# Optimization experiments

Measured on AMD Instinct MI355X. Metric: run time of the kernel, lower is better.

Reference implementation:

```python
import jax, jax.numpy as jnp
import numpy as np

N, E, B_GRAPHS = 50000, 512000, 64
XD, ED, C, H, L = 16, 8, 64, 2, 2
EPS = 1e-5


def setup_inputs() -> dict:
    key = jax.random.key(0)
    ks = jax.random.split(key, 20)
    w = lambda k, shape: jax.random.normal(k, shape, jnp.float32) * 0.1
    return {
        "x": jax.random.normal(ks[0], (N, XD), jnp.float32),
        "edge_attr": jax.random.normal(ks[1], (E, ED), jnp.float32),
        "edge_src": jax.random.randint(ks[2], (E,), 0, N, dtype=jnp.int32),
        "edge_dst": jax.random.randint(ks[3], (E,), 0, N, dtype=jnp.int32),
        "batch": jnp.sort(jax.random.randint(ks[4], (N,), 0, B_GRAPHS, dtype=jnp.int32)),
        "node_W": w(ks[5], (XD, C)), "node_b": jnp.zeros((C,), jnp.float32),
        "edge_W": w(ks[6], (ED, C)), "edge_b": jnp.zeros((C,), jnp.float32),
        "Wq": w(ks[7], (L, C, H * C)), "bq": jnp.zeros((L, H * C), jnp.float32),
        "Wk": w(ks[8], (L, C, H * C)), "bk": jnp.zeros((L, H * C), jnp.float32),
        "Wv": w(ks[9], (L, C, H * C)), "bv": jnp.zeros((L, H * C), jnp.float32),
        "We": w(ks[10], (L, C, H * C)), "be": jnp.zeros((L, H * C), jnp.float32),
        "Wskip": w(ks[11], (L, C, C)), "bskip": jnp.zeros((L, C), jnp.float32),
        "gamma": jnp.ones((L, C), jnp.float32), "beta": jnp.zeros((L, C), jnp.float32),
        "gate_W": w(ks[12], (C, 1)), "gate_b": jnp.zeros((1,), jnp.float32),
        "out_W": w(ks[13], (C, 1)), "out_b": jnp.zeros((1,), jnp.float32),
    }


def reference(x, edge_attr, edge_src, edge_dst, batch,
              node_W, node_b, edge_W, edge_b,
              Wq, bq, Wk, bk, Wv, bv, We, be,
              Wskip, bskip, gamma, beta,
              gate_W, gate_b, out_W, out_b):
    n = x.shape[0]
    h = x @ node_W + node_b                       # node encoder: [N, C]
    e = edge_attr @ edge_W + edge_b               # edge encoder: [E, C]
    scale = 1.0 / jnp.sqrt(jnp.float32(C))
    for i in range(L):
        identity = h
        # TransformerConv (UniMP), concat=False -> mean over heads
        q = (h @ Wq[i] + bq[i]).reshape(n, H, C)
        k = (h @ Wk[i] + bk[i]).reshape(n, H, C)
        v = (h @ Wv[i] + bv[i]).reshape(n, H, C)
        ep = (e @ We[i] + be[i]).reshape(-1, H, C)
        k_e = k[edge_src] + ep                    # [E, H, C]
        v_e = v[edge_src] + ep                    # [E, H, C]
        logits = jnp.einsum('ehc,ehc->eh', q[edge_dst], k_e) * scale
        # segment softmax over incoming edges of each target node
        m = jax.ops.segment_max(logits, edge_dst, num_segments=n)
        a = jnp.exp(logits - m[edge_dst])
        denom = jax.ops.segment_sum(a, edge_dst, num_segments=n)
        alpha = a / denom[edge_dst]               # [E, H]
        agg = jax.ops.segment_sum(alpha[:, :, None] * v_e, edge_dst, num_segments=n)
        out = agg.mean(axis=1) + h @ Wskip[i] + bskip[i]   # root/skip term
        # BatchNorm1d (training mode, biased variance)
        mu = out.mean(axis=0)
        var = out.var(axis=0)
        out = gamma[i] * (out - mu) * jax.lax.rsqrt(var + EPS) + beta[i]
        out = jax.nn.leaky_relu(out, 0.01)
        h = out + identity                        # residual
    # GlobalAttention pooling over graphs
    gate = (h @ gate_W + gate_b)[:, 0]            # [N]
    gm = jax.ops.segment_max(gate, batch, num_segments=B_GRAPHS)
    ge = jnp.exp(gate - gm[batch])
    gd = jax.ops.segment_sum(ge, batch, num_segments=B_GRAPHS)
    wts = ge / gd[batch]
    pooled = jax.ops.segment_sum(wts[:, None] * h, batch, num_segments=B_GRAPHS)
    return jax.nn.sigmoid(pooled @ out_W + out_b)  # [B_GRAPHS, 1]
```

## Files before the change

kernel.cpp:

```cpp
#include <hip/hip_runtime.h>
#include <hip/hip_bf16.h>

typedef unsigned short ushort_t;
typedef __attribute__((ext_vector_type(8))) short short8;
typedef __attribute__((ext_vector_type(4))) float float4v;

__device__ __forceinline__ float bfu_lo(unsigned u) {
    return __uint_as_float(u << 16);
}
__device__ __forceinline__ float bfu_hi(unsigned u) {
    return __uint_as_float(u & 0xffff0000u);
}
__device__ __forceinline__ ushort_t f2bf(float f) {
    __hip_bfloat16 h = __float2bfloat16(f);
    return *reinterpret_cast<ushort_t*>(&h);
}



__global__ __launch_bounds__(256) void setup_kernel(
    const float* __restrict__ x, const float* __restrict__ node_W,
    const float* __restrict__ node_b,
    const float* __restrict__ edge_W, const float* __restrict__ edge_b,
    const float* __restrict__ We, const float* __restrict__ be,
    const float* __restrict__ Wq, const float* __restrict__ bq,
    const float* __restrict__ Wk, const float* __restrict__ bk,
    const float* __restrict__ Wv, const float* __restrict__ bv,
    const float* __restrict__ Wskip, const float* __restrict__ bskip,
    float* __restrict__ h, ushort_t* __restrict__ h_bf,
    int* __restrict__ counts,
    float* __restrict__ Wc, float* __restrict__ bcb,
    ushort_t* __restrict__ Wall_arr, float* __restrict__ Wall_bias,
    int O0, int O1, int O2, int N) {
    int b = blockIdx.x, t = threadIdx.x;
    if (b < O0) {
        int idx = b * 256 + t;
        if (idx < N * 64) {
            int n = idx >> 6, c = idx & 63;
            float acc = node_b[c];
#pragma unroll
            for (int j = 0; j < 16; ++j) acc += x[n * 16 + j] * node_W[j * 64 + c];
            h[idx] = acc;
            h_bf[idx] = f2bf(acc);
        }
    } else if (b < O1) {
        int i = (b - O0) * 256 + t;
        if (i < N) counts[i] = 0;
    } else if (b < O2) {
        int tid = (b - O1) * 256 + t;
        if (tid < 2048) {
            int l = tid >> 10, d = (tid >> 7) & 7, j = tid & 127;
            float s = 0.f;
            for (int m = 0; m < 64; ++m) s += edge_W[d * 64 + m] * We[l * 8192 + m * 128 + j];
            Wc[l * 1024 + d * 128 + j] = s;
        } else if (tid < 2048 + 256) {
            int u = tid - 2048;
            int l = u >> 7, j = u & 127;
            float s = be[l * 128 + j];
            for (int m = 0; m < 64; ++m) s += edge_b[m] * We[l * 8192 + m * 128 + j];
            bcb[l * 128 + j] = s;
        }
    } else {
        int tid = (b - O2) * 256 + t;
        if (tid < 2 * 28672) {
            int l = tid / 28672, u = tid % 28672;
            int j = u & 7, ln = (u >> 3) & 63, kch = (u >> 9) & 1, ct = u >> 10;
            int nn = ln & 15, quad = ln >> 4;
            int k = kch * 32 + quad * 8 + j;
            int col = ct * 16 + nn;
            float v;
            if (col < 128)      v = Wq[l * 8192 + k * 128 + col];
            else if (col < 256) v = Wk[l * 8192 + k * 128 + col - 128];
            else if (col < 384) v = Wv[l * 8192 + k * 128 + col - 256];
            else                v = Wskip[l * 4096 + k * 64 + col - 384];
            Wall_arr[(size_t)l * 32768 + ct * 1024 + kch * 512 + ln * 8 + j] = f2bf(v);
        } else if (tid < 2 * 28672 + 2 * 448) {
            int u = tid - 2 * 28672;
            int l = u / 448, col = u % 448;
            float v;
            if (col < 128)      v = bq[l * 128 + col];
            else if (col < 256) v = bk[l * 128 + col - 128];
            else if (col < 384) v = bv[l * 128 + col - 256];
            else                v = bskip[l * 64 + col - 384];
            Wall_bias[l * 512 + col] = v;
        }
    }
}

__global__ void combine2_kernel(const float* __restrict__ Wq, const float* __restrict__ bq,
                                const float* __restrict__ Wc, const float* __restrict__ bcb,
                                ushort_t* __restrict__ Wall_arr, float* __restrict__ Wall_bias) {
    int tid = blockIdx.x * 256 + threadIdx.x;
    if (tid < 2304) {
        int l = tid / 1152, u = tid % 1152, k = u / 18, j = u % 18;
        float s = 0.f;
        if (j < 16) {
            int hh = j >> 3, d = j & 7;
            for (int c = 0; c < 64; ++c)
                s += Wq[l * 8192 + k * 128 + hh * 64 + c] * Wc[l * 1024 + d * 128 + hh * 64 + c];
        } else {
            int hh = j - 16;
            for (int c = 0; c < 64; ++c)
                s += Wq[l * 8192 + k * 128 + hh * 64 + c] * bcb[l * 128 + hh * 64 + c];
        }
        s *= 0.125f;
        int col = 448 + j;
        int ct = col >> 4, nn = col & 15;
        int kch = k >> 5, quad = (k >> 3) & 3, jj = k & 7;
        int ln = quad * 16 + nn;
        Wall_arr[(size_t)l * 32768 + ct * 1024 + kch * 512 + ln * 8 + jj] = f2bf(s);
    } else if (tid < 2304 + 36) {
        int u = tid - 2304;
        int l = u / 18, j = u % 18;
        float s = 0.f;
        if (j < 16) {
            int hh = j >> 3, d = j & 7;
            for (int c = 0; c < 64; ++c)
                s += bq[l * 128 + hh * 64 + c] * Wc[l * 1024 + d * 128 + hh * 64 + c];
        } else {
            int hh = j - 16;
            for (int c = 0; c < 64; ++c)
                s += bq[l * 128 + hh * 64 + c] * bcb[l * 128 + hh * 64 + c];
        }
        Wall_bias[l * 512 + 448 + j] = 0.125f * s;
    }
}


__global__ void csr_count_kernel(const int* __restrict__ dst, int* __restrict__ counts, int E) {
    int e = blockIdx.x * 256 + threadIdx.x;
    if (e < E) atomicAdd(&counts[dst[e]], 1);
}

__global__ void scan1_kernel(const int* __restrict__ counts, int* __restrict__ rowptr,
                             int* __restrict__ bsums, int N) {
    __shared__ int s[256];
    int t = threadIdx.x, i = blockIdx.x * 256 + t;
    int v = (i < N) ? counts[i] : 0;
    s[t] = v;
    __syncthreads();
    for (int d = 1; d < 256; d <<= 1) {
        int x = (t >= d) ? s[t - d] : 0;
        __syncthreads();
        s[t] += x;
        __syncthreads();
    }
    if (i < N) rowptr[i] = s[t] - v;
    if (t == 255) bsums[blockIdx.x] = s[255];
}

__global__ void scan3_kernel(int* __restrict__ rowptr, const int* __restrict__ bsums,
                             int* __restrict__ cursor, int N, int E, int nb) {
    __shared__ int sh[256];
    int t = threadIdx.x;
    int v = (t < nb) ? bsums[t] : 0;
    sh[t] = v;
    __syncthreads();
    for (int d = 1; d < 256; d <<= 1) {
        int x = (t >= d) ? sh[t - d] : 0;
        __syncthreads();
        sh[t] += x;
        __syncthreads();
    }
    int blk = blockIdx.x;
    int offv = (blk == 0) ? 0 : sh[blk - 1];
    int i = blk * 256 + t;
    if (i < N) {
        int r = rowptr[i] + offv;
        rowptr[i] = r;
        cursor[i] = r;
    }
    if (i == 0) rowptr[N] = E;
}

__global__ void csr_fill_kernel(const int* __restrict__ dst, const int* __restrict__ src,
                                const float* __restrict__ edge_attr, int* __restrict__ cursor,
                                int* __restrict__ csr_src, float* __restrict__ ea_perm, int E) {
    int e = blockIdx.x * 256 + threadIdx.x;
    if (e < E) {
        int pos = atomicAdd(&cursor[dst[e]], 1);
        csr_src[pos] = src[e] * 768 + 256;
        float4 a0 = *(const float4*)(edge_attr + (size_t)e * 8);
        float4 a1 = *(const float4*)(edge_attr + (size_t)e * 8 + 4);
        *(float4*)(ea_perm + (size_t)pos * 8) = a0;
        *(float4*)(ea_perm + (size_t)pos * 8 + 4) = a1;
    }
}


__global__ __launch_bounds__(256) void qkv_mfma_kernel(
    const ushort_t* __restrict__ h_bf,
    const ushort_t* __restrict__ Wall_arr, const float* __restrict__ Wall_bias,
    ushort_t* __restrict__ qkv, float* __restrict__ outbuf, float* __restrict__ qcbuf, int N) {
    int wave = threadIdx.x >> 6, lane = threadIdx.x & 63;
    int quad = lane >> 4, nn = lane & 15;
    int n0 = blockIdx.x * 32;
    int nodeA = n0 + nn;       if (nodeA >= N) nodeA = N - 1;
    int nodeB = n0 + 16 + nn;  if (nodeB >= N) nodeB = N - 1;
    const ushort_t* apA = h_bf + (size_t)nodeA * 64 + quad * 8;
    const ushort_t* apB = h_bf + (size_t)nodeB * 64 + quad * 8;
    short8 aA0 = *(const short8*)apA;
    short8 aA1 = *(const short8*)(apA + 32);
    short8 aB0 = *(const short8*)apB;
    short8 aB1 = *(const short8*)(apB + 32);
    int ct_start = (wave < 2) ? wave * 8 : (16 + (wave - 2) * 7);
    int ct_cnt = (wave < 2) ? 8 : 7;
    for (int i = 0; i < ct_cnt; ++i) {
        int ct = ct_start + i;
        const ushort_t* bp = Wall_arr + (size_t)ct * 1024 + lane * 8;
        short8 b0 = *(const short8*)bp;
        short8 b1 = *(const short8*)(bp + 512);
        float4v cA = {0.f, 0.f, 0.f, 0.f};
        float4v cB = {0.f, 0.f, 0.f, 0.f};
        cA = __builtin_amdgcn_mfma_f32_16x16x32_bf16(aA0, b0, cA, 0, 0, 0);
        cA = __builtin_amdgcn_mfma_f32_16x16x32_bf16(aA1, b1, cA, 0, 0, 0);
        cB = __builtin_amdgcn_mfma_f32_16x16x32_bf16(aB0, b0, cB, 0, 0, 0);
        cB = __builtin_amdgcn_mfma_f32_16x16x32_bf16(aB1, b1, cB, 0, 0, 0);
        int col = ct * 16 + nn;
        float bias = Wall_bias[col];
#pragma unroll
        for (int g = 0; g < 2; ++g) {
            float4v c = (g == 0) ? cA : cB;
            int nbase = n0 + g * 16 + quad * 4;
            if (col < 384) {
                int cm;
                if (col < 128) cm = col;
                else if (col < 256) { int cc = col - 128; cm = 128 + ((cc >> 1) << 2) + (cc & 1); }
                else { int cc = col - 256; cm = 128 + ((cc >> 1) << 2) + 2 + (cc & 1); }
                ushort_t* qp = qkv + (size_t)nbase * 384 + cm;
#pragma unroll
                for (int r = 0; r < 4; ++r)
                    if (nbase + r < N) qp[(size_t)r * 384] = f2bf(c[r] + bias);
            } else if (col < 448) {
                float* op = outbuf + (size_t)nbase * 64 + (col - 448 + 64);
#pragma unroll
                for (int r = 0; r < 4; ++r)
                    if (nbase + r < N) op[(size_t)r * 64] = c[r] + bias;
            } else if (col < 466) {
                float* qp2 = qcbuf + (size_t)nbase * 20 + (col - 448);
#pragma unroll
                for (int r = 0; r < 4; ++r)
                    if (nbase + r < N) qp2[(size_t)r * 20] = c[r] + bias;
            }
        }
    }
}


__global__ __launch_bounds__(256) void bnqkv_kernel(
    const float* __restrict__ outbuf_in, const float* __restrict__ bnsums,
    const float* __restrict__ gamma, const float* __restrict__ beta,
    float* __restrict__ h,
    const ushort_t* __restrict__ Wall_arr, const float* __restrict__ Wall_bias,
    ushort_t* __restrict__ qkv, float* __restrict__ outbuf, float* __restrict__ qcbuf, int N) {
    __shared__ ushort_t hb[32 * 64];
    __shared__ float ss_scale[64], ss_shift[64];
    int t = threadIdx.x;
    if (t < 64) {
        float invN = 1.f / (float)N;
        float mean = bnsums[t] * invN;
        float var = bnsums[64 + t] * invN - mean * mean;
        float sc = gamma[t] * rsqrtf(var + 1e-5f);
        ss_scale[t] = sc;
        ss_shift[t] = beta[t] - mean * sc;
    }
    __syncthreads();
    int n0 = blockIdx.x * 32;
    int c = t & 63;
    float sc = ss_scale[c], sh = ss_shift[c];
#pragma unroll
    for (int i = 0; i < 8; ++i) {
        int li = t + i * 256;
        int gidx = n0 * 64 + li;
        float hn = 0.f;
        if (gidx < N * 64) {
            float o = outbuf_in[gidx] * sc + sh;
            o = (o > 0.f) ? o : 0.01f * o;
            hn = h[gidx] + o;
            h[gidx] = hn;
        }
        hb[li] = f2bf(hn);
    }
    __syncthreads();
    int wave = t >> 6, lane = t & 63;
    int quad = lane >> 4, nn = lane & 15;
    const ushort_t* apA = hb + nn * 64 + quad * 8;
    const ushort_t* apB = hb + (16 + nn) * 64 + quad * 8;
    short8 aA0 = *(const short8*)apA;
    short8 aA1 = *(const short8*)(apA + 32);
    short8 aB0 = *(const short8*)apB;
    short8 aB1 = *(const short8*)(apB + 32);
    int ct_start = (wave < 2) ? wave * 8 : (16 + (wave - 2) * 7);
    int ct_cnt = (wave < 2) ? 8 : 7;
    for (int i = 0; i < ct_cnt; ++i) {
        int ct = ct_start + i;
        const ushort_t* bp = Wall_arr + (size_t)ct * 1024 + lane * 8;
        short8 b0 = *(const short8*)bp;
        short8 b1 = *(const short8*)(bp + 512);
        float4v cA = {0.f, 0.f, 0.f, 0.f};
        float4v cB = {0.f, 0.f, 0.f, 0.f};
        cA = __builtin_amdgcn_mfma_f32_16x16x32_bf16(aA0, b0, cA, 0, 0, 0);
        cA = __builtin_amdgcn_mfma_f32_16x16x32_bf16(aA1, b1, cA, 0, 0, 0);
        cB = __builtin_amdgcn_mfma_f32_16x16x32_bf16(aB0, b0, cB, 0, 0, 0);
        cB = __builtin_amdgcn_mfma_f32_16x16x32_bf16(aB1, b1, cB, 0, 0, 0);
        int col = ct * 16 + nn;
        float bias = Wall_bias[col];
#pragma unroll
        for (int g = 0; g < 2; ++g) {
            float4v cc2 = (g == 0) ? cA : cB;
            int nbase = n0 + g * 16 + quad * 4;
            if (col < 384) {
                int cm;
                if (col < 128) cm = col;
                else if (col < 256) { int cv = col - 128; cm = 128 + ((cv >> 1) << 2) + (cv & 1); }
                else { int cv = col - 256; cm = 128 + ((cv >> 1) << 2) + 2 + (cv & 1); }
                ushort_t* qp = qkv + (size_t)nbase * 384 + cm;
#pragma unroll
                for (int r = 0; r < 4; ++r)
                    if (nbase + r < N) qp[(size_t)r * 384] = f2bf(cc2[r] + bias);
            } else if (col < 448) {
                float* op = outbuf + (size_t)nbase * 64 + (col - 448 + 64);
#pragma unroll
                for (int r = 0; r < 4; ++r)
                    if (nbase + r < N) op[(size_t)r * 64] = cc2[r] + bias;
            } else if (col < 466) {
                float* qp2 = qcbuf + (size_t)nbase * 20 + (col - 448);
#pragma unroll
                for (int r = 0; r < 4; ++r)
                    if (nbase + r < N) qp2[(size_t)r * 20] = cc2[r] + bias;
            }
        }
    }
}


__global__ __launch_bounds__(256) void attn_kernel(
    const ushort_t* __restrict__ qkv, const float* __restrict__ qcbuf,
    const int* __restrict__ csr_src, const float* __restrict__ ea_perm,
    const int* __restrict__ rowptr,
    const float* __restrict__ Wc, const float* __restrict__ bcb,
    float* __restrict__ outbuf, float* __restrict__ part, int N) {
    __shared__ float Wc_s[1024];
    __shared__ float bc_s[128];
    __shared__ float stat[4][4][2][64];
    int t = threadIdx.x;
    for (int i = t; i < 1024; i += 256) Wc_s[i] = Wc[i];
    if (t < 128) bc_s[t] = bcb[t];
    {
        float* sf = &stat[0][0][0][0];
        for (int i = t; i < 2048; i += 256) sf[i] = 0.f;
    }
    __syncthreads();
    int lane = t & 63, wid = t >> 6;
    int grp = lane >> 4, l16 = lane & 15;
    int head = l16 >> 3, l8 = l16 & 7;
    const char* qkvb = (const char*)qkv;

    int n = blockIdx.x * 16 + wid * 4 + grp;
    bool active = (n < N);
    int nn = active ? n : (N - 1);
    int start = rowptr[nn];
    int end = rowptr[nn + 1];
    int deg = active ? (end - start) : 0;
    int wdeg = deg;
    wdeg = max(wdeg, __shfl_xor(wdeg, 16));
    wdeg = max(wdeg, __shfl_xor(wdeg, 32));

    float lsum = 0.f;
    float vacc[8] = {0.f, 0.f, 0.f, 0.f, 0.f, 0.f, 0.f, 0.f};
    float se[8]   = {0.f, 0.f, 0.f, 0.f, 0.f, 0.f, 0.f, 0.f};

    if (wdeg > 0) {
        uint4 qr = *(const uint4*)(qkvb + (size_t)nn * 768 + 16 * l16);
        float qf0 = bfu_lo(qr.x), qf1 = bfu_hi(qr.x);
        float qf2 = bfu_lo(qr.y), qf3 = bfu_hi(qr.y);
        float qf4 = bfu_lo(qr.z), qf5 = bfu_hi(qr.z);
        float qf6 = bfu_lo(qr.w), qf7 = bfu_hi(qr.w);
        const float* qcp = qcbuf + (size_t)nn * 20;
        float4 qcA = *(const float4*)(qcp + head * 8);
        float4 qcB = *(const float4*)(qcp + head * 8 + 4);
        float qb = qcp[16 + head];

        int offL = csr_src[(deg > 0) ? (start + min(l16, deg - 1)) : 0];
        int o0 = __shfl(offL, grp * 16);
        uint4 ca = *(const uint4*)(qkvb + (size_t)(unsigned)o0 + 32 * l16);
        uint4 cb = *(const uint4*)(qkvb + (size_t)(unsigned)o0 + 32 * l16 + 16);
        int gi0 = (deg > 0) ? start : 0;
        float4 e0 = *(const float4*)(ea_perm + (size_t)gi0 * 8);
        float4 e1 = *(const float4*)(ea_perm + (size_t)gi0 * 8 + 4);

        for (int it = 0; it < wdeg; ++it) {
            int itn = it + 1;
            if ((itn & 15) == 0) {
                offL = csr_src[(deg > 0) ? (start + min(itn + l16, deg - 1)) : 0];
            }
            int itc = min(itn, wdeg - 1);
            int on = __shfl(offL, grp * 16 + (itc & 15));
            uint4 na = *(const uint4*)(qkvb + (size_t)(unsigned)on + 32 * l16);
            uint4 nb2 = *(const uint4*)(qkvb + (size_t)(unsigned)on + 32 * l16 + 16);
            int gin = (deg > 0) ? (start + min(itc, deg - 1)) : 0;
            float4 f0 = *(const float4*)(ea_perm + (size_t)gin * 8);
            float4 f1 = *(const float4*)(ea_perm + (size_t)gin * 8 + 4);

            float dt = qf0 * bfu_lo(ca.x) + qf1 * bfu_hi(ca.x)
                     + qf2 * bfu_lo(ca.z) + qf3 * bfu_hi(ca.z)
                     + qf4 * bfu_lo(cb.x) + qf5 * bfu_hi(cb.x)
                     + qf6 * bfu_lo(cb.z) + qf7 * bfu_hi(cb.z);
            dt += __shfl_xor(dt, 1);
            dt += __shfl_xor(dt, 2);
            dt += __shfl_xor(dt, 4);
            float s0 = dt * 0.125f
                     + qcA.x * e0.x + qcA.y * e0.y + qcA.z * e0.z + qcA.w * e0.w
                     + qcB.x * e1.x + qcB.y * e1.y + qcB.z * e1.z + qcB.w * e1.w
                     + qb;
            float p = (it < deg) ? __expf(fmaxf(s0, -60.f)) : 0.f;
            lsum += p;
            vacc[0] += p * bfu_lo(ca.y); vacc[1] += p * bfu_hi(ca.y);
            vacc[2] += p * bfu_lo(ca.w); vacc[3] += p * bfu_hi(ca.w);
            vacc[4] += p * bfu_lo(cb.y); vacc[5] += p * bfu_hi(cb.y);
            vacc[6] += p * bfu_lo(cb.w); vacc[7] += p * bfu_hi(cb.w);
            se[0] += p * e0.x; se[1] += p * e0.y; se[2] += p * e0.z; se[3] += p * e0.w;
            se[4] += p * e1.x; se[5] += p * e1.y; se[6] += p * e1.z; se[7] += p * e1.w;
            ca = na; cb = nb2; e0 = f0; e1 = f1;
        }
    }

    if (active) {
        float inv = (deg > 0) ? (1.f / lsum) : 0.f;
        int jb = head * 64 + 8 * l8;
        float outv[8];
#pragma unroll
        for (int k2 = 0; k2 < 8; ++k2) {
            int j = jb + k2;
            float wv = lsum * bc_s[j];
#pragma unroll
            for (int m = 0; m < 8; ++m) wv += se[m] * Wc_s[m * 128 + j];
            float ox = (vacc[k2] + wv) * inv;
            float po = __shfl_xor(ox, 8);
            outv[k2] = 0.5f * (ox + po);
        }
        if (head == 0) {
            float* op = outbuf + (size_t)nn * 64 + 8 * l8;
            float4 c0 = *(const float4*)op;
            float4 c1 = *(const float4*)(op + 4);
            float fr[8];
            fr[0] = c0.x + outv[0]; fr[1] = c0.y + outv[1];
            fr[2] = c0.z + outv[2]; fr[3] = c0.w + outv[3];
            fr[4] = c1.x + outv[4]; fr[5] = c1.y + outv[5];
            fr[6] = c1.z + outv[6]; fr[7] = c1.w + outv[7];
            if (deg > 0) {
                *(float4*)op = make_float4(fr[0], fr[1], fr[2], fr[3]);
                *(float4*)(op + 4) = make_float4(fr[4], fr[5], fr[6], fr[7]);
            }
            float* sa = &stat[wid][grp][0][8 * l8];
            float* sq = &stat[wid][grp][1][8 * l8];
#pragma unroll
            for (int k2 = 0; k2 < 8; ++k2) {
                sa[k2] += fr[k2];
                sq[k2] += fr[k2] * fr[k2];
            }
        }
    }
    __syncthreads();
    if (t < 128) {
        int c = t & 63, qq = t >> 6;
        float s = 0.f;
#pragma unroll
        for (int w2 = 0; w2 < 4; ++w2)
#pragma unroll
            for (int g2 = 0; g2 < 4; ++g2) s += stat[w2][g2][qq][c];
        part[(size_t)blockIdx.x * 128 + t] = s;
    }
}


__global__ __launch_bounds__(256) void bnreduce_kernel(const float* __restrict__ part,
                                                       float* __restrict__ bnsums, int nb) {
    int s = blockIdx.x;
    int t = threadIdx.x;
    float a = 0.f;
    for (int b = t; b < nb; b += 256) a += part[(size_t)b * 128 + s];
    __shared__ float sh[256];
    sh[t] = a;
    __syncthreads();
    for (int d = 128; d; d >>= 1) {
        if (t < d) sh[t] += sh[t + d];
        __syncthreads();
    }
    if (t == 0) bnsums[s] = sh[0];
}

__global__ __launch_bounds__(256) void bnapply_kernel(
    const float* __restrict__ outbuf, const float* __restrict__ bnsums,
    const float* __restrict__ gamma, const float* __restrict__ beta,
    const float* __restrict__ gate_W, const float* __restrict__ gate_b,
    float* __restrict__ h, float* __restrict__ gatebuf, int N) {
    int idx = blockIdx.x * 256 + threadIdx.x;
    if (idx >= N * 64) return;
    int c = idx & 63, n = idx >> 6;
    float invN = 1.f / (float)N;
    float mean = bnsums[c] * invN;
    float var = bnsums[64 + c] * invN - mean * mean;
    float scale = gamma[c] * rsqrtf(var + 1e-5f);
    float shift = beta[c] - mean * scale;
    float o = outbuf[idx] * scale + shift;
    o = (o > 0.f) ? o : 0.01f * o;
    float hn = h[idx] + o;
    h[idx] = hn;
    float g = hn * gate_W[c];
#pragma unroll
    for (int off = 32; off; off >>= 1) g += __shfl_xor(g, off);
    if (c == 0) gatebuf[n] = g + gate_b[0];
}


__global__ __launch_bounds__(256) void pool_acc_kernel(
    const float* __restrict__ h, const float* __restrict__ gatebuf,
    const int* __restrict__ batch,
    float* __restrict__ pacc, float* __restrict__ pden, int N) {
    int b = blockIdx.x >> 3, chunk = blockIdx.x & 7;
    int lo = 0, hi = N;
    while (lo < hi) { int mid = (lo + hi) >> 1; if (batch[mid] < b) lo = mid + 1; else hi = mid; }
    int start = lo;
    lo = start; hi = N;
    while (lo < hi) { int mid = (lo + hi) >> 1; if (batch[mid] <= b) lo = mid + 1; else hi = mid; }
    int end = lo;
    int t = threadIdx.x, lane = t & 63, wid = t >> 6;
    __shared__ float sm[4];
    float mx = -1e30f;
    for (int n = start + t; n < end; n += 256) mx = fmaxf(mx, gatebuf[n]);
#pragma unroll
    for (int off = 32; off; off >>= 1) mx = fmaxf(mx, __shfl_xor(mx, off));
    if (lane == 0) sm[wid] = mx;
    __syncthreads();
    float mb = fmaxf(fmaxf(sm[0], sm[1]), fmaxf(sm[2], sm[3]));
    int gwid = chunk * 4 + wid;
    float acc = 0.f, den = 0.f;
    for (int n = start + gwid; n < end; n += 32) {
        float ge = __expf(gatebuf[n] - mb);
        acc += ge * h[(size_t)n * 64 + lane];
        den += ge;
    }
    __shared__ float sacc[4][64];
    __shared__ float sden[4];
    sacc[wid][lane] = acc;
    if (lane == 0) sden[wid] = den;
    __syncthreads();
    if (wid == 0) {
        pacc[(size_t)blockIdx.x * 64 + lane] =
            sacc[0][lane] + sacc[1][lane] + sacc[2][lane] + sacc[3][lane];
        if (lane == 0) pden[blockIdx.x] = sden[0] + sden[1] + sden[2] + sden[3];
    }
}

__global__ void pool_fin_kernel(const float* __restrict__ pacc, const float* __restrict__ pden,
                                const float* __restrict__ out_W, const float* __restrict__ out_b,
                                float* __restrict__ out) {
    int b = blockIdx.x, c = threadIdx.x;
    float pc = 0.f, dv = 0.f;
#pragma unroll
    for (int j = 0; j < 8; ++j) {
        pc += pacc[(size_t)(b * 8 + j) * 64 + c];
        dv += pden[b * 8 + j];
    }
    float s = pc * out_W[c];
#pragma unroll
    for (int off = 32; off; off >>= 1) s += __shfl_xor(s, off);
    if (c == 0) {
        if (dv <= 0.f) dv = 1.f;
        float v = s / dv + out_b[0];
        out[b] = 1.f / (1.f + __expf(-v));
    }
}


extern "C" void kernel_launch(void* const* d_in, const int* in_sizes, int n_in,
                              void* d_out, int out_size, void* d_ws, size_t ws_size,
                              hipStream_t stream) {
    const float* x         = (const float*)d_in[0];
    const float* edge_attr = (const float*)d_in[1];
    const int*   edge_src  = (const int*)d_in[2];
    const int*   edge_dst  = (const int*)d_in[3];
    const int*   batch     = (const int*)d_in[4];
    const float* node_W    = (const float*)d_in[5];
    const float* node_b    = (const float*)d_in[6];
    const float* edge_W    = (const float*)d_in[7];
    const float* edge_b    = (const float*)d_in[8];
    const float* Wq        = (const float*)d_in[9];
    const float* bq        = (const float*)d_in[10];
    const float* Wk        = (const float*)d_in[11];
    const float* bk        = (const float*)d_in[12];
    const float* Wv        = (const float*)d_in[13];
    const float* bv        = (const float*)d_in[14];
    const float* We        = (const float*)d_in[15];
    const float* be        = (const float*)d_in[16];
    const float* Wskip     = (const float*)d_in[17];
    const float* bskip     = (const float*)d_in[18];
    const float* gamma     = (const float*)d_in[19];
    const float* beta      = (const float*)d_in[20];
    const float* gate_W    = (const float*)d_in[21];
    const float* gate_b    = (const float*)d_in[22];
    const float* out_W     = (const float*)d_in[23];
    const float* out_b     = (const float*)d_in[24];
    float* out = (float*)d_out;

    const int N = in_sizes[0] / 16;
    const int E = in_sizes[2];
    const int nba = (N + 15) / 16;

    char* ws = (char*)d_ws;
    size_t off = 0;
    auto alloc = [&](size_t bytes) {
        size_t o = off;
        off += (bytes + 255) & ~(size_t)255;
        return o;
    };
    float*    h        = (float*)(ws + alloc((size_t)N * 64 * 4));
    ushort_t* h_bf     = (ushort_t*)(ws + alloc((size_t)N * 64 * 2));
    ushort_t* qkv      = (ushort_t*)(ws + alloc((size_t)N * 384 * 2));
    float*    outbuf   = (float*)(ws + alloc((size_t)N * 64 * 4));
    float*    qcbuf    = (float*)(ws + alloc((size_t)N * 20 * 4));
    int*      rowptr   = (int*)(ws + alloc((size_t)(N + 1) * 4));
    int*      cursor   = (int*)(ws + alloc((size_t)N * 4));
    int*      counts   = (int*)(ws + alloc((size_t)N * 4));
    int*      bsums    = (int*)(ws + alloc(1024));
    int*      csr_src  = (int*)(ws + alloc((size_t)E * 4));
    float*    ea_perm  = (float*)(ws + alloc((size_t)E * 8 * 4));
    float*    Wc       = (float*)(ws + alloc(2 * 1024 * 4));
    float*    bcb      = (float*)(ws + alloc(2 * 128 * 4));
    ushort_t* Wall_arr = (ushort_t*)(ws + alloc(2 * 32768 * 2));
    float*    Wall_b   = (float*)(ws + alloc(2 * 512 * 4));
    float*    bnsums   = (float*)(ws + alloc(128 * 4));
    float*    gatebuf  = (float*)(ws + alloc((size_t)N * 4));
    float*    pacc     = (float*)(ws + alloc((size_t)nba * 128 * 4));
    float*    pden     = (float*)(ws + alloc(512 * 4));
    if (off > ws_size) return;

    int O0 = (N * 64 + 255) / 256;
    int O1 = O0 + (N + 255) / 256;
    int O2 = O1 + 9;
    int O3 = O2 + 228;
    setup_kernel<<<O3, 256, 0, stream>>>(
        x, node_W, node_b, edge_W, edge_b, We, be, Wq, bq, Wk, bk, Wv, bv, Wskip, bskip,
        h, h_bf, counts, Wc, bcb, Wall_arr, Wall_b, O0, O1, O2, N);
    combine2_kernel<<<10, 256, 0, stream>>>(Wq, bq, Wc, bcb, Wall_arr, Wall_b);

    csr_count_kernel<<<(E + 255) / 256, 256, 0, stream>>>(edge_dst, counts, E);
    int nb = (N + 255) / 256;
    scan1_kernel<<<nb, 256, 0, stream>>>(counts, rowptr, bsums, N);
    scan3_kernel<<<nb, 256, 0, stream>>>(rowptr, bsums, cursor, N, E, nb);
    csr_fill_kernel<<<(E + 255) / 256, 256, 0, stream>>>(edge_dst, edge_src, edge_attr,
                                                         cursor, csr_src, ea_perm, E);

    qkv_mfma_kernel<<<(N + 31) / 32, 256, 0, stream>>>(
        h_bf, Wall_arr, Wall_b, qkv, outbuf, qcbuf, N);
    attn_kernel<<<nba, 256, 0, stream>>>(qkv, qcbuf, csr_src, ea_perm,
                                         rowptr, Wc, bcb, outbuf, pacc, N);
    bnreduce_kernel<<<128, 256, 0, stream>>>(pacc, bnsums, nba);
    bnqkv_kernel<<<(N + 31) / 32, 256, 0, stream>>>(
        outbuf, bnsums, gamma, beta, h,
        Wall_arr + 32768, Wall_b + 512, qkv, outbuf, qcbuf, N);

    attn_kernel<<<nba, 256, 0, stream>>>(qkv, qcbuf, csr_src, ea_perm,
                                         rowptr, Wc + 1024, bcb + 128,
                                         outbuf, pacc, N);
    bnreduce_kernel<<<128, 256, 0, stream>>>(pacc, bnsums, nba);
    bnapply_kernel<<<(N * 64 + 255) / 256, 256, 0, stream>>>(
        outbuf, bnsums, gamma + 64, beta + 64, gate_W, gate_b, h, gatebuf, N);

    pool_acc_kernel<<<512, 256, 0, stream>>>(h, gatebuf, batch, pacc, pden, N);
    pool_fin_kernel<<<64, 64, 0, stream>>>(pacc, pden, out_W, out_b, out);
}
```

Baseline: 383.2 us.

## Sort nodes by in-degree for attention scheduling and unroll edge loop by two

Builds a degree-bucketed permutation of nodes (histogram, scan, scatter) so each wavefront's four nodes have similar in-degree. This cuts wasted iterations from the per-wave max degree. The attention edge loop is also unrolled by two, prefetching two neighbours at once for more memory-level parallelism. The cost is extra small kernel launches, scattered per-node reads and writes through the permutation, and higher register pressure.

```diff
diff --git a/kernel.cpp b/kernel.cpp
--- a/kernel.cpp
+++ b/kernel.cpp
@@ -127,9 +127,41 @@
 }
 
 
-__global__ void csr_count_kernel(const int* __restrict__ dst, int* __restrict__ counts, int E) {
+__global__ void csr_count_kernel(const int* __restrict__ dst, int* __restrict__ counts,
+                                 int* __restrict__ hist, int E) {
+    if (blockIdx.x == 0 && threadIdx.x < 64) hist[threadIdx.x] = 0;
     int e = blockIdx.x * 256 + threadIdx.x;
     if (e < E) atomicAdd(&counts[dst[e]], 1);
+}
+
+__global__ void deg_hist_kernel(const int* __restrict__ counts, int* __restrict__ hist, int N) {
+    int n = blockIdx.x * 256 + threadIdx.x;
+    if (n < N) {
+        int b = 63 - min(counts[n], 63);
+        atomicAdd(&hist[b], 1);
+    }
+}
+
+__global__ void deg_scan_kernel(int* __restrict__ hist) {
+    int t = threadIdx.x;
+    int v = hist[t];
+    int s = v;
+#pragma unroll
+    for (int d = 1; d < 64; d <<= 1) {
+        int x = __shfl_up(s, d);
+        if (t >= d) s += x;
+    }
+    hist[t] = s - v;
+}
+
+__global__ void perm_scatter_kernel(const int* __restrict__ counts, int* __restrict__ hist,
+                                    int* __restrict__ perm, int N) {
+    int n = blockIdx.x * 256 + threadIdx.x;
+    if (n < N) {
+        int b = 63 - min(counts[n], 63);
+        int pos = atomicAdd(&hist[b], 1);
+        perm[pos] = n;
+    }
 }
 
 __global__ void scan1_kernel(const int* __restrict__ counts, int* __restrict__ rowptr,
@@ -337,7 +369,7 @@
 __global__ __launch_bounds__(256) void attn_kernel(
     const ushort_t* __restrict__ qkv, const float* __restrict__ qcbuf,
     const int* __restrict__ csr_src, const float* __restrict__ ea_perm,
-    const int* __restrict__ rowptr,
+    const int* __restrict__ rowptr, const int* __restrict__ perm,
     const float* __restrict__ Wc, const float* __restrict__ bcb,
     float* __restrict__ outbuf, float* __restrict__ part, int N) {
     __shared__ float Wc_s[1024];
@@ -356,12 +388,11 @@
     int head = l16 >> 3, l8 = l16 & 7;
     const char* qkvb = (const char*)qkv;
 
-    int n = blockIdx.x * 16 + wid * 4 + grp;
-    bool active = (n < N);
-    int nn = active ? n : (N - 1);
+    int slot = blockIdx.x * 16 + wid * 4 + grp;
+    bool active = (slot < N);
+    int nn = perm[active ? slot : (N - 1)];
     int start = rowptr[nn];
-    int end = rowptr[nn + 1];
-    int deg = active ? (end - start) : 0;
+    int deg = active ? (rowptr[nn + 1] - start) : 0;
     int wdeg = deg;
     wdeg = max(wdeg, __shfl_xor(wdeg, 16));
     wdeg = max(wdeg, __shfl_xor(wdeg, 32));
@@ -381,47 +412,84 @@
         float4 qcB = *(const float4*)(qcp + head * 8 + 4);
         float qb = qcp[16 + head];
 
-        int offL = csr_src[(deg > 0) ? (start + min(l16, deg - 1)) : 0];
+        bool dpos = (deg > 0);
+        int dclamp = dpos ? (deg - 1) : 0;
+
+        int offL = csr_src[dpos ? (start + min(l16, dclamp)) : 0];
+
+        int i1 = min(1, wdeg - 1);
         int o0 = __shfl(offL, grp * 16);
-        uint4 ca = *(const uint4*)(qkvb + (size_t)(unsigned)o0 + 32 * l16);
-        uint4 cb = *(const uint4*)(qkvb + (size_t)(unsigned)o0 + 32 * l16 + 16);
-        int gi0 = (deg > 0) ? start : 0;
-        float4 e0 = *(const float4*)(ea_perm + (size_t)gi0 * 8);
-        float4 e1 = *(const float4*)(ea_perm + (size_t)gi0 * 8 + 4);
-
-        for (int it = 0; it < wdeg; ++it) {
-            int itn = it + 1;
-            if ((itn & 15) == 0) {
-                offL = csr_src[(deg > 0) ? (start + min(itn + l16, deg - 1)) : 0];
-            }
-            int itc = min(itn, wdeg - 1);
-            int on = __shfl(offL, grp * 16 + (itc & 15));
-            uint4 na = *(const uint4*)(qkvb + (size_t)(unsigned)on + 32 * l16);
-            uint4 nb2 = *(const uint4*)(qkvb + (size_t)(unsigned)on + 32 * l16 + 16);
-            int gin = (deg > 0) ? (start + min(itc, deg - 1)) : 0;
-            float4 f0 = *(const float4*)(ea_perm + (size_t)gin * 8);
-            float4 f1 = *(const float4*)(ea_perm + (size_t)gin * 8 + 4);
-
-            float dt = qf0 * bfu_lo(ca.x) + qf1 * bfu_hi(ca.x)
-                     + qf2 * bfu_lo(ca.z) + qf3 * bfu_hi(ca.z)
-                     + qf4 * bfu_lo(cb.x) + qf5 * bfu_hi(cb.x)
-                     + qf6 * bfu_lo(cb.z) + qf7 * bfu_hi(cb.z);
-            dt += __shfl_xor(dt, 1);
-            dt += __shfl_xor(dt, 2);
-            dt += __shfl_xor(dt, 4);
-            float s0 = dt * 0.125f
-                     + qcA.x * e0.x + qcA.y * e0.y + qcA.z * e0.z + qcA.w * e0.w
-                     + qcB.x * e1.x + qcB.y * e1.y + qcB.z * e1.z + qcB.w * e1.w
-                     + qb;
-            float p = (it < deg) ? __expf(fmaxf(s0, -60.f)) : 0.f;
-            lsum += p;
-            vacc[0] += p * bfu_lo(ca.y); vacc[1] += p * bfu_hi(ca.y);
-            vacc[2] += p * bfu_lo(ca.w); vacc[3] += p * bfu_hi(ca.w);
-            vacc[4] += p * bfu_lo(cb.y); vacc[5] += p * bfu_hi(cb.y);
-            vacc[6] += p * bfu_lo(cb.w); vacc[7] += p * bfu_hi(cb.w);
-            se[0] += p * e0.x; se[1] += p * e0.y; se[2] += p * e0.z; se[3] += p * e0.w;
-            se[4] += p * e1.x; se[5] += p * e1.y; se[6] += p * e1.z; se[7] += p * e1.w;
-            ca = na; cb = nb2; e0 = f0; e1 = f1;
+        int o1 = __shfl(offL, grp * 16 + i1);
+        uint4 ca0 = *(const uint4*)(qkvb + (size_t)(unsigned)o0 + 32 * l16);
+        uint4 cb0 = *(const uint4*)(qkvb + (size_t)(unsigned)o0 + 32 * l16 + 16);
+        uint4 ca1 = *(const uint4*)(qkvb + (size_t)(unsigned)o1 + 32 * l16);
+        uint4 cb1 = *(const uint4*)(qkvb + (size_t)(unsigned)o1 + 32 * l16 + 16);
+        int g0 = dpos ? start : 0;
+        int g1 = dpos ? (start + min(i1, dclamp)) : 0;
+        float4 e00 = *(const float4*)(ea_perm + (size_t)g0 * 8);
+        float4 e01 = *(const float4*)(ea_perm + (size_t)g0 * 8 + 4);
+        float4 e10 = *(const float4*)(ea_perm + (size_t)g1 * 8);
+        float4 e11 = *(const float4*)(ea_perm + (size_t)g1 * 8 + 4);
+
+        for (int it = 0; it < wdeg; it += 2) {
+            int p0 = it + 2;
+            if ((p0 & 15) == 0 && p0 < wdeg)
+                offL = csr_src[dpos ? (start + min(p0 + l16, dclamp)) : 0];
+            int q0 = min(p0, wdeg - 1);
+            int q1 = min(p0 + 1, wdeg - 1);
+            int on0 = __shfl(offL, grp * 16 + (q0 & 15));
+            int on1 = __shfl(offL, grp * 16 + (q1 & 15));
+            uint4 na0 = *(const uint4*)(qkvb + (size_t)(unsigned)on0 + 32 * l16);
+            uint4 nb0 = *(const uint4*)(qkvb + (size_t)(unsigned)on0 + 32 * l16 + 16);
+            uint4 na1 = *(const uint4*)(qkvb + (size_t)(unsigned)on1 + 32 * l16);
+            uint4 nb1 = *(const uint4*)(qkvb + (size_t)(unsigned)on1 + 32 * l16 + 16);
+            int gn0 = dpos ? (start + min(q0, dclamp)) : 0;
+            int gn1 = dpos ? (start + min(q1, dclamp)) : 0;
+            float4 f00 = *(const float4*)(ea_perm + (size_t)gn0 * 8);
+            float4 f01 = *(const float4*)(ea_perm + (size_t)gn0 * 8 + 4);
+            float4 f10 = *(const float4*)(ea_perm + (size_t)gn1 * 8);
+            float4 f11 = *(const float4*)(ea_perm + (size_t)gn1 * 8 + 4);
+
+            float dt0 = qf0 * bfu_lo(ca0.x) + qf1 * bfu_hi(ca0.x)
+                      + qf2 * bfu_lo(ca0.z) + qf3 * bfu_hi(ca0.z)
+                      + qf4 * bfu_lo(cb0.x) + qf5 * bfu_hi(cb0.x)
+                      + qf6 * bfu_lo(cb0.z) + qf7 * bfu_hi(cb0.z);
+            float dt1 = qf0 * bfu_lo(ca1.x) + qf1 * bfu_hi(ca1.x)
+                      + qf2 * bfu_lo(ca1.z) + qf3 * bfu_hi(ca1.z)
+                      + qf4 * bfu_lo(cb1.x) + qf5 * bfu_hi(cb1.x)
+                      + qf6 * bfu_lo(cb1.z) + qf7 * bfu_hi(cb1.z);
+            dt0 += __shfl_xor(dt0, 1); dt1 += __shfl_xor(dt1, 1);
+            dt0 += __shfl_xor(dt0, 2); dt1 += __shfl_xor(dt1, 2);
+            dt0 += __shfl_xor(dt0, 4); dt1 += __shfl_xor(dt1, 4);
+            float s00 = dt0 * 0.125f
+                      + qcA.x * e00.x + qcA.y * e00.y + qcA.z * e00.z + qcA.w * e00.w
+                      + qcB.x * e01.x + qcB.y * e01.y + qcB.z * e01.z + qcB.w * e01.w
+                      + qb;
+            float s01 = dt1 * 0.125f
+                      + qcA.x * e10.x + qcA.y * e10.y + qcA.z * e10.z + qcA.w * e10.w
+                      + qcB.x * e11.x + qcB.y * e11.y + qcB.z * e11.z + qcB.w * e11.w
+                      + qb;
+            float p0v = (it < deg) ? __expf(fmaxf(s00, -60.f)) : 0.f;
+            float p1v = (it + 1 < deg) ? __expf(fmaxf(s01, -60.f)) : 0.f;
+            lsum += p0v + p1v;
+            vacc[0] += p0v * bfu_lo(ca0.y) + p1v * bfu_lo(ca1.y);
+            vacc[1] += p0v * bfu_hi(ca0.y) + p1v * bfu_hi(ca1.y);
+            vacc[2] += p0v * bfu_lo(ca0.w) + p1v * bfu_lo(ca1.w);
+            vacc[3] += p0v * bfu_hi(ca0.w) + p1v * bfu_hi(ca1.w);
+            vacc[4] += p0v * bfu_lo(cb0.y) + p1v * bfu_lo(cb1.y);
+            vacc[5] += p0v * bfu_hi(cb0.y) + p1v * bfu_hi(cb1.y);
+            vacc[6] += p0v * bfu_lo(cb0.w) + p1v * bfu_lo(cb1.w);
+            vacc[7] += p0v * bfu_hi(cb0.w) + p1v * bfu_hi(cb1.w);
+            se[0] += p0v * e00.x + p1v * e10.x;
+            se[1] += p0v * e00.y + p1v * e10.y;
+            se[2] += p0v * e00.z + p1v * e10.z;
+            se[3] += p0v * e00.w + p1v * e10.w;
+            se[4] += p0v * e01.x + p1v * e11.x;
+            se[5] += p0v * e01.y + p1v * e11.y;
+            se[6] += p0v * e01.z + p1v * e11.z;
+            se[7] += p0v * e01.w + p1v * e11.w;
+            ca0 = na0; cb0 = nb0; ca1 = na1; cb1 = nb1;
+            e00 = f00; e01 = f01; e10 = f10; e11 = f11;
         }
     }
 
@@ -634,6 +702,8 @@
     float*    gatebuf  = (float*)(ws + alloc((size_t)N * 4));
     float*    pacc     = (float*)(ws + alloc((size_t)nba * 128 * 4));
     float*    pden     = (float*)(ws + alloc(512 * 4));
+    int*      hist     = (int*)(ws + alloc(256));
+    int*      perm     = (int*)(ws + alloc((size_t)N * 4));
     if (off > ws_size) return;
 
     int O0 = (N * 64 + 255) / 256;
@@ -645,24 +715,27 @@
         h, h_bf, counts, Wc, bcb, Wall_arr, Wall_b, O0, O1, O2, N);
     combine2_kernel<<<10, 256, 0, stream>>>(Wq, bq, Wc, bcb, Wall_arr, Wall_b);
 
-    csr_count_kernel<<<(E + 255) / 256, 256, 0, stream>>>(edge_dst, counts, E);
+    csr_count_kernel<<<(E + 255) / 256, 256, 0, stream>>>(edge_dst, counts, hist, E);
+    deg_hist_kernel<<<(N + 255) / 256, 256, 0, stream>>>(counts, hist, N);
     int nb = (N + 255) / 256;
     scan1_kernel<<<nb, 256, 0, stream>>>(counts, rowptr, bsums, N);
     scan3_kernel<<<nb, 256, 0, stream>>>(rowptr, bsums, cursor, N, E, nb);
+    deg_scan_kernel<<<1, 64, 0, stream>>>(hist);
     csr_fill_kernel<<<(E + 255) / 256, 256, 0, stream>>>(edge_dst, edge_src, edge_attr,
                                                          cursor, csr_src, ea_perm, E);
+    perm_scatter_kernel<<<(N + 255) / 256, 256, 0, stream>>>(counts, hist, perm, N);
 
     qkv_mfma_kernel<<<(N + 31) / 32, 256, 0, stream>>>(
         h_bf, Wall_arr, Wall_b, qkv, outbuf, qcbuf, N);
     attn_kernel<<<nba, 256, 0, stream>>>(qkv, qcbuf, csr_src, ea_perm,
-                                         rowptr, Wc, bcb, outbuf, pacc, N);
+                                         rowptr, perm, Wc, bcb, outbuf, pacc, N);
     bnreduce_kernel<<<128, 256, 0, stream>>>(pacc, bnsums, nba);
     bnqkv_kernel<<<(N + 31) / 32, 256, 0, stream>>>(
         outbuf, bnsums, gamma, beta, h,
         Wall_arr + 32768, Wall_b + 512, qkv, outbuf, qcbuf, N);
 
     attn_kernel<<<nba, 256, 0, stream>>>(qkv, qcbuf, csr_src, ea_perm,
-                                         rowptr, Wc + 1024, bcb + 128,
+                                         rowptr, perm, Wc + 1024, bcb + 128,
                                          outbuf, pacc, N);
     bnreduce_kernel<<<128, 256, 0, stream>>>(pacc, bnsums, nba);
     bnapply_kernel<<<(N * 64 + 255) / 256, 256, 0, stream>>>(
```

Measured after the change: 720.3 us. 87.9% more time.
